# Kernel tuning notes

Hardware: AMD Instinct MI355X
Metric: run time of the kernel (lower is better)

Reference implementation:

```python
import jax, jax.numpy as jnp
import numpy as np
from jax import lax

MEM_SLOTS = 100
DECAY = 0.9


def setup_inputs() -> dict:
    key = jax.random.key(0)
    k1, k2, k3 = jax.random.split(key, 3)
    feats = jax.random.normal(k1, (32, 512, 64, 64), dtype=jnp.float32)
    preds = jax.random.uniform(k2, (32, 1, 64, 64), dtype=jnp.float32)
    W = jax.random.normal(k3, (256, 512), dtype=jnp.float32) * 0.02
    b = jnp.zeros((256,), dtype=jnp.float32)
    return {"feats": feats, "preds": preds, "W": W, "b": b, "epoch": 20}


def _update_memory(pooled, threshold):
    """Sequential codebook update: cosine-sim match -> EMA update or append.
    pooled: [B, C]. Returns (memory [100, C], ptr int32)."""
    C = pooled.shape[1]
    slot_ids = jnp.arange(MEM_SLOTS)

    def step(carry, x):
        memory, ptr = carry
        xn = x / jnp.linalg.norm(x)
        norms = jnp.linalg.norm(memory, axis=-1, keepdims=True)
        mem_n = memory / jnp.where(norms == 0, 1.0, norms)
        sims = mem_n @ xn                                   # [100]
        sims = jnp.where(slot_ids < ptr, sims, -jnp.inf)
        idx = jnp.argmax(sims)
        val = sims[idx]
        do_ema = (ptr > 0) & (val >= threshold)
        ema_mem = memory.at[idx].set(memory[idx] * DECAY + (1.0 - DECAY) * x)
        app_mem = memory.at[ptr].set(x)
        new_mem = jnp.where(do_ema, ema_mem, app_mem)
        new_ptr = jnp.where(do_ema, ptr, ptr + 1)
        return (new_mem, new_ptr), None

    init = (jnp.zeros((MEM_SLOTS, C), pooled.dtype), jnp.int32(0))
    (memory, ptr), _ = lax.scan(step, init, pooled)
    return memory, ptr


def reference(feats, preds, W, b, epoch):
    # 1x1 conv projection 512 -> 256
    proj = jnp.einsum('oc,bchw->bohw', W, feats) + b[None, :, None, None]
    B, C, H, Wd = proj.shape
    HW = H * Wd

    # dynamic threshold (epoch % 10 == 0 in original schedule)
    threshold = (epoch / 10 - 2) * 0.4 / 13 + 0.3

    # masked average pooling (no-grad path in original)
    pooled = jnp.mean(lax.stop_gradient(proj).reshape(B, C, HW)
                      * preds.reshape(B, 1, HW), axis=-1)   # [B, C]
    memory, ptr = _update_memory(pooled, threshold)
    memory = lax.stop_gradient(memory)                      # buffer, no grad

    # memory cross-attention over valid slots only
    key_ = proj.reshape(B, C, HW)
    logit = jnp.einsum('pc,bcl->bpl', memory, key_)         # [B, 100, HW]
    valid = (jnp.arange(MEM_SLOTS) < ptr)[None, :, None]
    logit = jnp.where(valid, logit, -jnp.inf)
    attn = jax.nn.softmax(logit, axis=1)                    # softmax over slots
    aug = jnp.einsum('bpl,pc->bcl', attn, memory).reshape(B, C, H, Wd)
    return jnp.concatenate([proj, aug], axis=1)             # [B, 512, H, W]
```

## Files before the change

kernel.cpp:

```cpp
#include <hip/hip_runtime.h>
#include <math.h>

#define CH_IN   512
#define CH_OUT  256
#define HWD     4096
#define BATCH   32
#define MAXSLOT 32

typedef __attribute__((ext_vector_type(8))) short short8;
typedef __attribute__((ext_vector_type(4))) float floatx4;

__device__ __forceinline__ unsigned int pk_bf16(float a, float b) {
    unsigned int ua = __float_as_uint(a);
    ua += 0x7fffu + ((ua >> 16) & 1u);
    unsigned int ub = __float_as_uint(b);
    ub += 0x7fffu + ((ub >> 16) & 1u);
    return (ua >> 16) | (ub & 0xffff0000u);
}

#define PA 40
#define PB 42
__global__ __launch_bounds__(256) void k1_proj_gemm(
    const float* __restrict__ feats, const float* __restrict__ preds,
    const float* __restrict__ W, const float* __restrict__ bias,
    float* __restrict__ out, float* __restrict__ pooled)
{
    __shared__ __align__(16) unsigned short As[128 * PA];
    __shared__ __align__(16) unsigned short Bs[128 * PB];

    const int t  = threadIdx.x;
    const int bid  = blockIdx.x;
    const int xcd  = bid & 7;
    const int slot = bid >> 3;
    const int tile = xcd * 128 + (slot >> 1);
    const int ot   = slot & 1;
    const int lt   = tile & 31;
    const int b    = tile >> 5;

    const int l0 = lt * 128, o0 = ot * 128;
    const int lane = t & 63, wid = t >> 6;
    const int wm = wid & 1, wn = wid >> 1;
    const int ln = lane & 15, quad = lane >> 4;

    floatx4 acc[4][4];
    #pragma unroll
    for (int i = 0; i < 4; i++)
        #pragma unroll
        for (int j = 0; j < 4; j++) acc[i][j] = (floatx4){0.f, 0.f, 0.f, 0.f};

    const float* Wb = W + (size_t)o0 * CH_IN;
    const float* Fb = feats + (size_t)b * CH_IN * HWD + l0;

    const int l4 = t & 31;
    const int cg = t >> 5;

    for (int k0 = 0; k0 < CH_IN; k0 += 32) {
        #pragma unroll
        for (int q = 0; q < 4; q++) {
            int idx = t + 256 * q;
            int o = idx >> 3, c4 = idx & 7;
            float4 w = *(const float4*)(Wb + (size_t)o * CH_IN + k0 + c4 * 4);
            unsigned int u0 = pk_bf16(w.x, w.y);
            unsigned int u1 = pk_bf16(w.z, w.w);
            *(uint2*)(As + o * PA + c4 * 4) = make_uint2(u0, u1);
        }
        float4 f0 = *(const float4*)(Fb + (size_t)(k0 + cg * 4 + 0) * HWD + l4 * 4);
        float4 f1 = *(const float4*)(Fb + (size_t)(k0 + cg * 4 + 1) * HWD + l4 * 4);
        float4 f2 = *(const float4*)(Fb + (size_t)(k0 + cg * 4 + 2) * HWD + l4 * 4);
        float4 f3 = *(const float4*)(Fb + (size_t)(k0 + cg * 4 + 3) * HWD + l4 * 4);
        {
            const float v0[4] = {f0.x, f0.y, f0.z, f0.w};
            const float v1[4] = {f1.x, f1.y, f1.z, f1.w};
            const float v2[4] = {f2.x, f2.y, f2.z, f2.w};
            const float v3[4] = {f3.x, f3.y, f3.z, f3.w};
            #pragma unroll
            for (int i = 0; i < 4; i++) {
                unsigned short* row = Bs + (l4 * 4 + i) * PB + cg * 4;
                *(unsigned int*)(row)     = pk_bf16(v0[i], v1[i]);
                *(unsigned int*)(row + 2) = pk_bf16(v2[i], v3[i]);
            }
        }
        __syncthreads();

        short8 af[4], bf[4];
        #pragma unroll
        for (int mt = 0; mt < 4; mt++) {
            int row = wm * 64 + mt * 16 + ln;
            af[mt] = *(const short8*)(As + row * PA + quad * 8);
        }
        #pragma unroll
        for (int nt = 0; nt < 4; nt++) {
            int row = wn * 64 + nt * 16 + ln;
            const unsigned short* p = Bs + row * PB + quad * 8;
            union { short8 v; unsigned int u[4]; } r;
            r.u[0] = *(const unsigned int*)(p);
            r.u[1] = *(const unsigned int*)(p + 2);
            r.u[2] = *(const unsigned int*)(p + 4);
            r.u[3] = *(const unsigned int*)(p + 6);
            bf[nt] = r.v;
        }
        #pragma unroll
        for (int mt = 0; mt < 4; mt++)
            #pragma unroll
            for (int nt = 0; nt < 4; nt++)
                acc[mt][nt] = __builtin_amdgcn_mfma_f32_16x16x32_bf16(
                    af[mt], bf[nt], acc[mt][nt], 0, 0, 0);
        __syncthreads();
    }

    float pv[4];
    #pragma unroll
    for (int nt = 0; nt < 4; nt++)
        pv[nt] = preds[(size_t)b * HWD + l0 + wn * 64 + nt * 16 + ln];

    #pragma unroll
    for (int mt = 0; mt < 4; mt++) {
        #pragma unroll
        for (int r = 0; r < 4; r++) {
            int o = o0 + wm * 64 + mt * 16 + quad * 4 + r;
            float bv = bias[o];
            float* op = out + ((size_t)b * 512 + o) * HWD + l0 + wn * 64;
            float psum = 0.f;
            #pragma unroll
            for (int nt = 0; nt < 4; nt++) {
                float val = acc[mt][nt][r] + bv;
                op[nt * 16 + ln] = val;
                psum += val * pv[nt];
            }
            #pragma unroll
            for (int off = 1; off < 16; off <<= 1)
                psum += __shfl_xor(psum, off, 64);
            if (ln == 0)
                atomicAdd(&pooled[(size_t)b * CH_OUT + o], psum);
        }
    }
}

__global__ __launch_bounds__(1024) void k2_mem_update(
    const float* __restrict__ pooled, const int* __restrict__ epoch_p,
    float* __restrict__ mem_out, int* __restrict__ ptr_out)
{
    __shared__ float mem[MAXSLOT][256];
    __shared__ float xs[256];
    __shared__ float norms2[MAXSLOT];
    __shared__ float sims[MAXSLOT];
    __shared__ float red[4];
    __shared__ float xnorm2_s;
    __shared__ int ptr_s, row_s, ema_s;

    const int t = threadIdx.x;
    const int lane = t & 63, wid = t >> 6;

    if (t < 256)
        for (int r = 0; r < MAXSLOT; r++) mem[r][t] = 0.f;
    if (t < MAXSLOT) norms2[t] = 0.f;
    if (t == 0) ptr_s = 0;

    double thr_d = ((double)(*epoch_p)) / 10.0 - 2.0;
    thr_d = thr_d * 0.4 / 13.0 + 0.3;
    const float thr = (float)thr_d;
    __syncthreads();

    for (int bi = 0; bi < BATCH; bi++) {
        if (t < 256) {
            float x = pooled[(size_t)bi * 256 + t] * (1.0f / 4096.0f);
            xs[t] = x;
            float s = x * x;
            #pragma unroll
            for (int off = 32; off >= 1; off >>= 1) s += __shfl_xor(s, off, 64);
            if (lane == 0) red[wid] = s;
        }
        __syncthreads();
        if (t == 0) xnorm2_s = red[0] + red[1] + red[2] + red[3];
        __syncthreads();

        const int P = ptr_s;
        const float xn = sqrtf(xnorm2_s);
        for (int p = wid; p < P; p += 16) {
            float d = mem[p][lane]       * xs[lane]
                    + mem[p][lane + 64]  * xs[lane + 64]
                    + mem[p][lane + 128] * xs[lane + 128]
                    + mem[p][lane + 192] * xs[lane + 192];
            #pragma unroll
            for (int off = 32; off >= 1; off >>= 1) d += __shfl_xor(d, off, 64);
            if (lane == 0) {
                float nrm = sqrtf(norms2[p]);
                if (nrm == 0.f) nrm = 1.f;
                sims[p] = d / (nrm * xn);
            }
        }
        __syncthreads();

        if (wid == 0) {
            float v = (lane < P) ? sims[lane] : -INFINITY;
            int idx = lane;
            #pragma unroll
            for (int off = 32; off >= 1; off >>= 1) {
                float ov = __shfl_down(v, off, 64);
                int   oi = __shfl_down(idx, off, 64);
                if (ov > v || (ov == v && oi < idx)) { v = ov; idx = oi; }
            }
            if (lane == 0) {
                int ema = (P > 0 && v >= thr) ? 1 : 0;
                ema_s = ema;
                row_s = ema ? idx : P;
                if (!ema) ptr_s = P + 1;
            }
        }
        __syncthreads();

        const int r = row_s;
        if (t < 256) {
            float nv = ema_s ? (mem[r][t] * 0.9f + 0.1f * xs[t]) : xs[t];
            mem[r][t] = nv;
            float s2 = nv * nv;
            #pragma unroll
            for (int off = 32; off >= 1; off >>= 1) s2 += __shfl_xor(s2, off, 64);
            if (lane == 0) red[wid] = s2;
        }
        __syncthreads();
        if (t == 0) norms2[r] = red[0] + red[1] + red[2] + red[3];
        __syncthreads();
    }

    if (t < 256)
        for (int r = 0; r < MAXSLOT; r++) mem_out[(size_t)r * 256 + t] = mem[r][t];
    if (t == 0) ptr_out[0] = ptr_s;
}

#define PM 260
#define PT 132
__global__ __launch_bounds__(256) void k3_attention(
    const float* __restrict__ mem_g, const int* __restrict__ ptr_g,
    float* __restrict__ out)
{
    __shared__ __align__(16) float memL[MAXSLOT * PM];
    __shared__ __align__(16) float attnL[MAXSLOT * PT];

    const int t = threadIdx.x;
    const int lt = blockIdx.x, b = blockIdx.y;
    const int l0 = lt * 128;
    const int P = ptr_g[0];

    #pragma unroll
    for (int q = 0; q < 8; q++) {
        int idx = t + 256 * q;
        int p = idx >> 6, c4 = idx & 63;
        *(float4*)(memL + p * PM + c4 * 4) =
            *(const float4*)(mem_g + (size_t)p * 256 + c4 * 4);
    }
    __syncthreads();

    {
        const int tx = t & 15;
        const int py = t >> 4;
        const int p0 = py * 2;
        const int sl4 = t & 31;
        const int scw = t >> 5;

        const float* projB = out + (size_t)b * 512 * HWD + l0;
        float a0[8], a1[8];
        #pragma unroll
        for (int j = 0; j < 8; j++) { a0[j] = 0.f; a1[j] = 0.f; }
        const float* m0p = memL + p0 * PM;
        const float* m1p = memL + (p0 + 1) * PM;

        float4 st[4];
        #pragma unroll
        for (int q = 0; q < 4; q++)
            st[q] = *(const float4*)(projB + (size_t)(scw + q * 8) * HWD + sl4 * 4);

        for (int c0 = 0; c0 < 256; c0 += 32) {
            __syncthreads();
            #pragma unroll
            for (int q = 0; q < 4; q++)
                *(float4*)(attnL + (scw + q * 8) * PT + sl4 * 4) = st[q];
            __syncthreads();
            if (c0 + 32 < 256) {
                #pragma unroll
                for (int q = 0; q < 4; q++)
                    st[q] = *(const float4*)(projB +
                        (size_t)(c0 + 32 + scw + q * 8) * HWD + sl4 * 4);
            }
            #pragma unroll 4
            for (int cc = 0; cc < 32; cc++) {
                const int c = c0 + cc;
                const float* sp = attnL + cc * PT + tx * 8;
                float4 pA = *(const float4*)(sp);
                float4 pB = *(const float4*)(sp + 4);
                float m0 = m0p[c], m1 = m1p[c];
                a0[0] = fmaf(m0, pA.x, a0[0]); a1[0] = fmaf(m1, pA.x, a1[0]);
                a0[1] = fmaf(m0, pA.y, a0[1]); a1[1] = fmaf(m1, pA.y, a1[1]);
                a0[2] = fmaf(m0, pA.z, a0[2]); a1[2] = fmaf(m1, pA.z, a1[2]);
                a0[3] = fmaf(m0, pA.w, a0[3]); a1[3] = fmaf(m1, pA.w, a1[3]);
                a0[4] = fmaf(m0, pB.x, a0[4]); a1[4] = fmaf(m1, pB.x, a1[4]);
                a0[5] = fmaf(m0, pB.y, a0[5]); a1[5] = fmaf(m1, pB.y, a1[5]);
                a0[6] = fmaf(m0, pB.z, a0[6]); a1[6] = fmaf(m1, pB.z, a1[6]);
                a0[7] = fmaf(m0, pB.w, a0[7]); a1[7] = fmaf(m1, pB.w, a1[7]);
            }
        }
        __syncthreads();
        #pragma unroll
        for (int j = 0; j < 8; j++) {
            attnL[p0 * PT + tx * 8 + j]       = a0[j];
            attnL[(p0 + 1) * PT + tx * 8 + j] = a1[j];
        }
    }
    __syncthreads();

    if (t < 128) {
        float m = -INFINITY;
        for (int p = 0; p < P; p++) m = fmaxf(m, attnL[p * PT + t]);
        float d = 0.f;
        for (int p = 0; p < P; p++) {
            float e = __expf(attnL[p * PT + t] - m);
            attnL[p * PT + t] = e;
            d += e;
        }
        float inv = 1.f / d;
        for (int p = 0; p < P; p++) attnL[p * PT + t] *= inv;
    }
    __syncthreads();

    {
        const int lC = t & 127;
        const int h = t >> 7;
        const int c0 = h * 128;
        float ar[MAXSLOT];
        for (int p = 0; p < P; p++) ar[p] = attnL[p * PT + lC];

        float* augB = out + ((size_t)b * 512 + 256 + c0) * HWD + l0 + lC;
        for (int cc = 0; cc < 128; cc += 8) {
            float acc[8];
            #pragma unroll
            for (int j = 0; j < 8; j++) acc[j] = 0.f;
            for (int p = 0; p < P; p++) {
                float4 mA = *(const float4*)(memL + p * PM + c0 + cc);
                float4 mB = *(const float4*)(memL + p * PM + c0 + cc + 4);
                float a = ar[p];
                acc[0] = fmaf(a, mA.x, acc[0]);
                acc[1] = fmaf(a, mA.y, acc[1]);
                acc[2] = fmaf(a, mA.z, acc[2]);
                acc[3] = fmaf(a, mA.w, acc[3]);
                acc[4] = fmaf(a, mB.x, acc[4]);
                acc[5] = fmaf(a, mB.y, acc[5]);
                acc[6] = fmaf(a, mB.z, acc[6]);
                acc[7] = fmaf(a, mB.w, acc[7]);
            }
            #pragma unroll
            for (int j = 0; j < 8; j++)
                augB[(size_t)(cc + j) * HWD] = acc[j];
        }
    }
}

extern "C" void kernel_launch(void* const* d_in, const int* in_sizes, int n_in,
                              void* d_out, int out_size, void* d_ws, size_t ws_size,
                              hipStream_t stream) {
    const float* feats = (const float*)d_in[0];
    const float* preds = (const float*)d_in[1];
    const float* W     = (const float*)d_in[2];
    const float* bias  = (const float*)d_in[3];
    const int*   epoch = (const int*)d_in[4];
    float* out = (float*)d_out;

    float* ws     = (float*)d_ws;
    float* pooled = ws;
    float* mem_g  = ws + 8192;
    int*   ptr_g  = (int*)(ws + 16384);

    hipMemsetAsync(pooled, 0, 8192 * sizeof(float), stream);

    k1_proj_gemm<<<dim3(2048), 256, 0, stream>>>(feats, preds, W, bias, out, pooled);
    k2_mem_update<<<1, 1024, 0, stream>>>(pooled, epoch, mem_g, ptr_g);
    k3_attention<<<dim3(32, 32), 256, 0, stream>>>(mem_g, ptr_g, out);
}
```

Measured before the change: 659.0 us.

## Read memory codebook from global/cache instead of LDS and retile attention logits

The codebook copy into shared memory is removed, and both attention phases now read memory rows straight from global memory. Wave-uniform addresses may let these become scalar loads or L1 hits. The logit micro-tile changes from 2 slots x 8 columns to 4 slots x 4 columns, with float4 loads of memory values over 4 channels. The aggregation phase reads attention weights from LDS directly instead of a per-thread register array that could spill. This cuts LDS footprint and the staging sync, but trades LDS reads for global/cache loads in the inner loops.

```diff
diff --git a/kernel.cpp b/kernel.cpp
--- a/kernel.cpp
+++ b/kernel.cpp
@@ -228,13 +228,18 @@
     if (t == 0) ptr_out[0] = ptr_s;
 }
 
-#define PM 260
 #define PT 132
+
+#define K3_FMA4(MI, PV, AI) \
+    AI[0] = fmaf(MI, PV.x, AI[0]); \
+    AI[1] = fmaf(MI, PV.y, AI[1]); \
+    AI[2] = fmaf(MI, PV.z, AI[2]); \
+    AI[3] = fmaf(MI, PV.w, AI[3]);
+
 __global__ __launch_bounds__(256) void k3_attention(
     const float* __restrict__ mem_g, const int* __restrict__ ptr_g,
     float* __restrict__ out)
 {
-    __shared__ __align__(16) float memL[MAXSLOT * PM];
     __shared__ __align__(16) float attnL[MAXSLOT * PT];
 
     const int t = threadIdx.x;
@@ -242,28 +247,22 @@
     const int l0 = lt * 128;
     const int P = ptr_g[0];
 
-    #pragma unroll
-    for (int q = 0; q < 8; q++) {
-        int idx = t + 256 * q;
-        int p = idx >> 6, c4 = idx & 63;
-        *(float4*)(memL + p * PM + c4 * 4) =
-            *(const float4*)(mem_g + (size_t)p * 256 + c4 * 4);
-    }
-    __syncthreads();
-
     {
-        const int tx = t & 15;
-        const int py = t >> 4;
-        const int p0 = py * 2;
+        const int tx = t & 31;
+        const int py = t >> 5;
+        const int p0 = py * 4;
         const int sl4 = t & 31;
         const int scw = t >> 5;
 
         const float* projB = out + (size_t)b * 512 * HWD + l0;
-        float a0[8], a1[8];
-        #pragma unroll
-        for (int j = 0; j < 8; j++) { a0[j] = 0.f; a1[j] = 0.f; }
-        const float* m0p = memL + p0 * PM;
-        const float* m1p = memL + (p0 + 1) * PM;
+        float a0[4], a1[4], a2[4], a3[4];
+        #pragma unroll
+        for (int j = 0; j < 4; j++) { a0[j] = 0.f; a1[j] = 0.f; a2[j] = 0.f; a3[j] = 0.f; }
+
+        const float* m0p = mem_g + (size_t)(p0 + 0) * 256;
+        const float* m1p = mem_g + (size_t)(p0 + 1) * 256;
+        const float* m2p = mem_g + (size_t)(p0 + 2) * 256;
+        const float* m3p = mem_g + (size_t)(p0 + 3) * 256;
 
         float4 st[4];
         #pragma unroll
@@ -282,28 +281,42 @@
                     st[q] = *(const float4*)(projB +
                         (size_t)(c0 + 32 + scw + q * 8) * HWD + sl4 * 4);
             }
-            #pragma unroll 4
-            for (int cc = 0; cc < 32; cc++) {
+            #pragma unroll 2
+            for (int cc = 0; cc < 32; cc += 4) {
                 const int c = c0 + cc;
-                const float* sp = attnL + cc * PT + tx * 8;
-                float4 pA = *(const float4*)(sp);
-                float4 pB = *(const float4*)(sp + 4);
-                float m0 = m0p[c], m1 = m1p[c];
-                a0[0] = fmaf(m0, pA.x, a0[0]); a1[0] = fmaf(m1, pA.x, a1[0]);
-                a0[1] = fmaf(m0, pA.y, a0[1]); a1[1] = fmaf(m1, pA.y, a1[1]);
-                a0[2] = fmaf(m0, pA.z, a0[2]); a1[2] = fmaf(m1, pA.z, a1[2]);
-                a0[3] = fmaf(m0, pA.w, a0[3]); a1[3] = fmaf(m1, pA.w, a1[3]);
-                a0[4] = fmaf(m0, pB.x, a0[4]); a1[4] = fmaf(m1, pB.x, a1[4]);
-                a0[5] = fmaf(m0, pB.y, a0[5]); a1[5] = fmaf(m1, pB.y, a1[5]);
-                a0[6] = fmaf(m0, pB.z, a0[6]); a1[6] = fmaf(m1, pB.z, a1[6]);
-                a0[7] = fmaf(m0, pB.w, a0[7]); a1[7] = fmaf(m1, pB.w, a1[7]);
-            }
-        }
-        __syncthreads();
-        #pragma unroll
-        for (int j = 0; j < 8; j++) {
-            attnL[p0 * PT + tx * 8 + j]       = a0[j];
-            attnL[(p0 + 1) * PT + tx * 8 + j] = a1[j];
+                float4 m0 = *(const float4*)(m0p + c);
+                float4 m1 = *(const float4*)(m1p + c);
+                float4 m2 = *(const float4*)(m2p + c);
+                float4 m3 = *(const float4*)(m3p + c);
+                {
+                    float4 pv = *(const float4*)(attnL + (cc + 0) * PT + tx * 4);
+                    K3_FMA4(m0.x, pv, a0) K3_FMA4(m1.x, pv, a1)
+                    K3_FMA4(m2.x, pv, a2) K3_FMA4(m3.x, pv, a3)
+                }
+                {
+                    float4 pv = *(const float4*)(attnL + (cc + 1) * PT + tx * 4);
+                    K3_FMA4(m0.y, pv, a0) K3_FMA4(m1.y, pv, a1)
+                    K3_FMA4(m2.y, pv, a2) K3_FMA4(m3.y, pv, a3)
+                }
+                {
+                    float4 pv = *(const float4*)(attnL + (cc + 2) * PT + tx * 4);
+                    K3_FMA4(m0.z, pv, a0) K3_FMA4(m1.z, pv, a1)
+                    K3_FMA4(m2.z, pv, a2) K3_FMA4(m3.z, pv, a3)
+                }
+                {
+                    float4 pv = *(const float4*)(attnL + (cc + 3) * PT + tx * 4);
+                    K3_FMA4(m0.w, pv, a0) K3_FMA4(m1.w, pv, a1)
+                    K3_FMA4(m2.w, pv, a2) K3_FMA4(m3.w, pv, a3)
+                }
+            }
+        }
+        __syncthreads();
+        #pragma unroll
+        for (int j = 0; j < 4; j++) {
+            attnL[(p0 + 0) * PT + tx * 4 + j] = a0[j];
+            attnL[(p0 + 1) * PT + tx * 4 + j] = a1[j];
+            attnL[(p0 + 2) * PT + tx * 4 + j] = a2[j];
+            attnL[(p0 + 3) * PT + tx * 4 + j] = a3[j];
         }
     }
     __syncthreads();
@@ -326,8 +339,8 @@
         const int lC = t & 127;
         const int h = t >> 7;
         const int c0 = h * 128;
-        float ar[MAXSLOT];
-        for (int p = 0; p < P; p++) ar[p] = attnL[p * PT + lC];
+        const float* attC = attnL + lC;
+        const float* memB = mem_g + c0;
 
         float* augB = out + ((size_t)b * 512 + 256 + c0) * HWD + l0 + lC;
         for (int cc = 0; cc < 128; cc += 8) {
@@ -335,9 +348,9 @@
             #pragma unroll
             for (int j = 0; j < 8; j++) acc[j] = 0.f;
             for (int p = 0; p < P; p++) {
-                float4 mA = *(const float4*)(memL + p * PM + c0 + cc);
-                float4 mB = *(const float4*)(memL + p * PM + c0 + cc + 4);
-                float a = ar[p];
+                float4 mA = *(const float4*)(memB + (size_t)p * 256 + cc);
+                float4 mB = *(const float4*)(memB + (size_t)p * 256 + cc + 4);
+                float a = attC[p * PT];
                 acc[0] = fmaf(a, mA.x, acc[0]);
                 acc[1] = fmaf(a, mA.y, acc[1]);
                 acc[2] = fmaf(a, mA.z, acc[2]);
```

After: 734.0 us. +11.4%, slower.

## Move attention logit and aggregation GEMMs to bf16 MFMA in k3

Applied to the files above, without the earlier changes.

Rewrites the attention kernel so the memory-by-projection logits and the attention-by-memory aggregation both run on bf16 16x16x32 MFMA instructions instead of scalar FP32 FMAs. Memory slots and projection tiles are converted to bf16 and staged in padded shared buffers, and the aggregation is fixed at 32 slots with zero-padded attention. This cuts ALU work and the per-thread register loops. In exchange it adds bf16 rounding error in the logits and the output, and the shared-memory layout for the second GEMM is rebuilt by re-reading memory from global.

```diff
diff --git a/kernel.cpp b/kernel.cpp
--- a/kernel.cpp
+++ b/kernel.cpp
@@ -228,13 +228,15 @@
     if (t == 0) ptr_out[0] = ptr_s;
 }
 
-#define PM 260
-#define PT 132
+#define PT  132
+#define PMS 40
+#define PBS 42
 __global__ __launch_bounds__(256) void k3_attention(
     const float* __restrict__ mem_g, const int* __restrict__ ptr_g,
     float* __restrict__ out)
 {
-    __shared__ __align__(16) float memL[MAXSLOT * PM];
+    __shared__ __align__(16) unsigned short memS[10240];
+    __shared__ __align__(16) unsigned short Bs[128 * PBS];
     __shared__ __align__(16) float attnL[MAXSLOT * PT];
 
     const int t = threadIdx.x;
@@ -242,70 +244,69 @@
     const int l0 = lt * 128;
     const int P = ptr_g[0];
 
-    #pragma unroll
-    for (int q = 0; q < 8; q++) {
+    const int lane = t & 63, wid = t >> 6;
+    const int wm = wid & 1, wn = wid >> 1;
+    const int ln = lane & 15, quad = lane >> 4;
+
+    #pragma unroll
+    for (int q = 0; q < 16; q++) {
         int idx = t + 256 * q;
-        int p = idx >> 6, c4 = idx & 63;
-        *(float4*)(memL + p * PM + c4 * 4) =
-            *(const float4*)(mem_g + (size_t)p * 256 + c4 * 4);
-    }
-    __syncthreads();
-
-    {
-        const int tx = t & 15;
-        const int py = t >> 4;
-        const int p0 = py * 2;
-        const int sl4 = t & 31;
-        const int scw = t >> 5;
-
-        const float* projB = out + (size_t)b * 512 * HWD + l0;
-        float a0[8], a1[8];
-        #pragma unroll
-        for (int j = 0; j < 8; j++) { a0[j] = 0.f; a1[j] = 0.f; }
-        const float* m0p = memL + p0 * PM;
-        const float* m1p = memL + (p0 + 1) * PM;
-
-        float4 st[4];
-        #pragma unroll
-        for (int q = 0; q < 4; q++)
-            st[q] = *(const float4*)(projB + (size_t)(scw + q * 8) * HWD + sl4 * 4);
-
-        for (int c0 = 0; c0 < 256; c0 += 32) {
-            __syncthreads();
-            #pragma unroll
-            for (int q = 0; q < 4; q++)
-                *(float4*)(attnL + (scw + q * 8) * PT + sl4 * 4) = st[q];
-            __syncthreads();
-            if (c0 + 32 < 256) {
-                #pragma unroll
-                for (int q = 0; q < 4; q++)
-                    st[q] = *(const float4*)(projB +
-                        (size_t)(c0 + 32 + scw + q * 8) * HWD + sl4 * 4);
-            }
-            #pragma unroll 4
-            for (int cc = 0; cc < 32; cc++) {
-                const int c = c0 + cc;
-                const float* sp = attnL + cc * PT + tx * 8;
-                float4 pA = *(const float4*)(sp);
-                float4 pB = *(const float4*)(sp + 4);
-                float m0 = m0p[c], m1 = m1p[c];
-                a0[0] = fmaf(m0, pA.x, a0[0]); a1[0] = fmaf(m1, pA.x, a1[0]);
-                a0[1] = fmaf(m0, pA.y, a0[1]); a1[1] = fmaf(m1, pA.y, a1[1]);
-                a0[2] = fmaf(m0, pA.z, a0[2]); a1[2] = fmaf(m1, pA.z, a1[2]);
-                a0[3] = fmaf(m0, pA.w, a0[3]); a1[3] = fmaf(m1, pA.w, a1[3]);
-                a0[4] = fmaf(m0, pB.x, a0[4]); a1[4] = fmaf(m1, pB.x, a1[4]);
-                a0[5] = fmaf(m0, pB.y, a0[5]); a1[5] = fmaf(m1, pB.y, a1[5]);
-                a0[6] = fmaf(m0, pB.z, a0[6]); a1[6] = fmaf(m1, pB.z, a1[6]);
-                a0[7] = fmaf(m0, pB.w, a0[7]); a1[7] = fmaf(m1, pB.w, a1[7]);
-            }
-        }
-        __syncthreads();
-        #pragma unroll
-        for (int j = 0; j < 8; j++) {
-            attnL[p0 * PT + tx * 8 + j]       = a0[j];
-            attnL[(p0 + 1) * PT + tx * 8 + j] = a1[j];
-        }
-    }
+        int p = idx >> 7, cp = idx & 127;
+        float2 v = *(const float2*)(mem_g + (size_t)p * 256 + cp * 2);
+        *(unsigned int*)(memS + (cp >> 4) * (32 * PMS) + p * PMS + (cp & 15) * 2)
+            = pk_bf16(v.x, v.y);
+    }
+
+    const float* Pb = out + (size_t)b * 512 * HWD + l0;
+    const int l4 = t & 31;
+    const int cg = t >> 5;
+
+    floatx4 accA[4];
+    #pragma unroll
+    for (int nt = 0; nt < 4; nt++) accA[nt] = (floatx4){0.f, 0.f, 0.f, 0.f};
+
+    for (int k0 = 0; k0 < 8; k0++) {
+        float4 f0 = *(const float4*)(Pb + (size_t)(k0 * 32 + cg * 4 + 0) * HWD + l4 * 4);
+        float4 f1 = *(const float4*)(Pb + (size_t)(k0 * 32 + cg * 4 + 1) * HWD + l4 * 4);
+        float4 f2 = *(const float4*)(Pb + (size_t)(k0 * 32 + cg * 4 + 2) * HWD + l4 * 4);
+        float4 f3 = *(const float4*)(Pb + (size_t)(k0 * 32 + cg * 4 + 3) * HWD + l4 * 4);
+        {
+            const float v0[4] = {f0.x, f0.y, f0.z, f0.w};
+            const float v1[4] = {f1.x, f1.y, f1.z, f1.w};
+            const float v2[4] = {f2.x, f2.y, f2.z, f2.w};
+            const float v3[4] = {f3.x, f3.y, f3.z, f3.w};
+            #pragma unroll
+            for (int i = 0; i < 4; i++) {
+                unsigned short* row = Bs + (l4 * 4 + i) * PBS + cg * 4;
+                *(unsigned int*)(row)     = pk_bf16(v0[i], v1[i]);
+                *(unsigned int*)(row + 2) = pk_bf16(v2[i], v3[i]);
+            }
+        }
+        __syncthreads();
+
+        short8 af = *(const short8*)(memS + k0 * (32 * PMS) + (wm * 16 + ln) * PMS + quad * 8);
+        short8 bf[4];
+        #pragma unroll
+        for (int nt = 0; nt < 4; nt++) {
+            const unsigned short* p = Bs + (wn * 64 + nt * 16 + ln) * PBS + quad * 8;
+            union { short8 v; unsigned int u[4]; } r;
+            r.u[0] = *(const unsigned int*)(p);
+            r.u[1] = *(const unsigned int*)(p + 2);
+            r.u[2] = *(const unsigned int*)(p + 4);
+            r.u[3] = *(const unsigned int*)(p + 6);
+            bf[nt] = r.v;
+        }
+        #pragma unroll
+        for (int nt = 0; nt < 4; nt++)
+            accA[nt] = __builtin_amdgcn_mfma_f32_16x16x32_bf16(af, bf[nt], accA[nt], 0, 0, 0);
+        __syncthreads();
+    }
+
+    #pragma unroll
+    for (int nt = 0; nt < 4; nt++)
+        #pragma unroll
+        for (int r = 0; r < 4; r++)
+            attnL[(wm * 16 + quad * 4 + r) * PT + wn * 64 + nt * 16 + ln] = accA[nt][r];
     __syncthreads();
 
     if (t < 128) {
@@ -322,34 +323,56 @@
     }
     __syncthreads();
 
-    {
-        const int lC = t & 127;
-        const int h = t >> 7;
-        const int c0 = h * 128;
-        float ar[MAXSLOT];
-        for (int p = 0; p < P; p++) ar[p] = attnL[p * PT + lC];
-
-        float* augB = out + ((size_t)b * 512 + 256 + c0) * HWD + l0 + lC;
-        for (int cc = 0; cc < 128; cc += 8) {
-            float acc[8];
-            #pragma unroll
-            for (int j = 0; j < 8; j++) acc[j] = 0.f;
-            for (int p = 0; p < P; p++) {
-                float4 mA = *(const float4*)(memL + p * PM + c0 + cc);
-                float4 mB = *(const float4*)(memL + p * PM + c0 + cc + 4);
-                float a = ar[p];
-                acc[0] = fmaf(a, mA.x, acc[0]);
-                acc[1] = fmaf(a, mA.y, acc[1]);
-                acc[2] = fmaf(a, mA.z, acc[2]);
-                acc[3] = fmaf(a, mA.w, acc[3]);
-                acc[4] = fmaf(a, mB.x, acc[4]);
-                acc[5] = fmaf(a, mB.y, acc[5]);
-                acc[6] = fmaf(a, mB.z, acc[6]);
-                acc[7] = fmaf(a, mB.w, acc[7]);
-            }
-            #pragma unroll
-            for (int j = 0; j < 8; j++)
-                augB[(size_t)(cc + j) * HWD] = acc[j];
+    if (t < 128) {
+        #pragma unroll
+        for (int pp = 0; pp < 16; pp++) {
+            float a = (2 * pp     < P) ? attnL[(2 * pp) * PT + t]     : 0.f;
+            float c = (2 * pp + 1 < P) ? attnL[(2 * pp + 1) * PT + t] : 0.f;
+            *(unsigned int*)(Bs + t * PBS + pp * 2) = pk_bf16(a, c);
+        }
+    }
+    #pragma unroll
+    for (int q = 0; q < 16; q++) {
+        int idx = t + 256 * q;
+        int c = idx & 255, pp = idx >> 8;
+        float va = mem_g[(size_t)(2 * pp)     * 256 + c];
+        float vb = mem_g[(size_t)(2 * pp + 1) * 256 + c];
+        *(unsigned int*)(memS + c * PMS + pp * 2) = pk_bf16(va, vb);
+    }
+    __syncthreads();
+
+    short8 bfc[4];
+    #pragma unroll
+    for (int nt = 0; nt < 4; nt++) {
+        const unsigned short* p = Bs + (wn * 64 + nt * 16 + ln) * PBS + quad * 8;
+        union { short8 v; unsigned int u[4]; } r;
+        r.u[0] = *(const unsigned int*)(p);
+        r.u[1] = *(const unsigned int*)(p + 2);
+        r.u[2] = *(const unsigned int*)(p + 4);
+        r.u[3] = *(const unsigned int*)(p + 6);
+        bfc[nt] = r.v;
+    }
+    const floatx4 zf = (floatx4){0.f, 0.f, 0.f, 0.f};
+    for (int h = 0; h < 2; h++) {
+        const int cbase = h * 128 + wm * 64;
+        short8 afc[4];
+        #pragma unroll
+        for (int ct = 0; ct < 4; ct++)
+            afc[ct] = *(const short8*)(memS + (cbase + ct * 16 + ln) * PMS + quad * 8);
+        #pragma unroll
+        for (int ct = 0; ct < 4; ct++) {
+            floatx4 accC[4];
+            #pragma unroll
+            for (int nt = 0; nt < 4; nt++)
+                accC[nt] = __builtin_amdgcn_mfma_f32_16x16x32_bf16(afc[ct], bfc[nt], zf, 0, 0, 0);
+            #pragma unroll
+            for (int r = 0; r < 4; r++) {
+                int c = cbase + ct * 16 + quad * 4 + r;
+                float* op = out + ((size_t)b * 512 + 256 + c) * HWD + l0 + wn * 64;
+                #pragma unroll
+                for (int nt = 0; nt < 4; nt++)
+                    op[nt * 16 + ln] = accC[nt][r];
+            }
         }
     }
 }
```

Measured after the change: 592.8 us. 10.0% less time.
